# Kernel optimization log

Measured on AMD Instinct MI355X. Metric: run time of the kernel, lower is better.

The kernel has to match this reference:

```python
import jax, jax.numpy as jnp
import numpy as np
import math

H = 1024
NH = 16
D = H // NH  # 64
EPS = 1e-5


def _layernorm(x, g, b):
    mu = jnp.mean(x, axis=-1, keepdims=True)
    var = jnp.mean(jnp.square(x - mu), axis=-1, keepdims=True)
    return (x - mu) * jax.lax.rsqrt(var + EPS) * g + b


def setup_inputs() -> dict:
    key = jax.random.key(0)
    ks = jax.random.split(key, 12)
    B, T = 2, 2048
    q = jax.random.normal(ks[0], (B, T, H), jnp.float32)
    k = jax.random.normal(ks[1], (B, T, H), jnp.float32)
    v = jax.random.normal(ks[2], (B, T, H), jnp.float32)
    pad_mask = jax.random.randint(ks[3], (B, T), 0, 2) > 0
    s = 0.02
    Wq = jax.random.normal(ks[4], (H, H), jnp.float32) * s
    Wk = jax.random.normal(ks[5], (H, H), jnp.float32) * s
    Wv = jax.random.normal(ks[6], (H, H), jnp.float32) * s
    Wo = jax.random.normal(ks[7], (H, H), jnp.float32) * s
    W1 = jax.random.normal(ks[8], (4 * H, H), jnp.float32) * s
    b1 = jnp.zeros((4 * H,), jnp.float32)
    W2 = jax.random.normal(ks[9], (H, 4 * H), jnp.float32) * s
    b2 = jnp.zeros((H,), jnp.float32)
    g1 = jnp.ones((H,), jnp.float32); be1 = jnp.zeros((H,), jnp.float32)
    g2 = jnp.ones((H,), jnp.float32); be2 = jnp.zeros((H,), jnp.float32)
    return dict(q=q, k=k, v=v, pad_mask=pad_mask, Wq=Wq, Wk=Wk, Wv=Wv, Wo=Wo,
                W1=W1, b1=b1, W2=W2, b2=b2, g1=g1, be1=be1, g2=g2, be2=be2)


def reference(q, k, v, pad_mask, Wq, Wk, Wv, Wo, W1, b1, W2, b2, g1, be1, g2, be2):
    B, Tq, _ = q.shape
    Tv = v.shape[1]
    # torch nn.Linear: x @ W.T
    Q = (q @ Wq.T).reshape(B, NH, Tq, D)  # faithful to torch .view head split
    K = (k @ Wk.T).reshape(B, NH, Tv, D)
    V = (v @ Wv.T).reshape(B, NH, Tv, D)
    logits = jnp.einsum('baih,bajh->baij', Q, K)  # [B,NH,Tq,Tv]
    neg_inf = jnp.float32(-jnp.inf)
    logits = jnp.where(pad_mask[:, None, None, :], logits, neg_inf)
    attn = jax.nn.softmax(logits / math.sqrt(D), axis=-1)
    # post-softmax query-mask multiply (custom)
    attn = attn * pad_mask[:, None, :, None].astype(attn.dtype)
    h = jnp.einsum('baij,bajh->baih', attn, V).reshape(B, Tq, H)
    h = h @ Wo.T
    h = _layernorm(q + h, g1, be1)
    ff = jax.nn.gelu(h @ W1.T + b1, approximate=False) @ W2.T + b2  # dropout = identity (eval)
    return _layernorm(h + ff, g2, be2)
```

## Files before the change

### kernel.cpp

```cpp
#include <hip/hip_runtime.h>

typedef unsigned short u16;
typedef unsigned int u32;
typedef __attribute__((ext_vector_type(8))) __bf16 bf16x8;
typedef __attribute__((ext_vector_type(4))) float f32x4;
typedef __attribute__((ext_vector_type(16))) float f32x16;
typedef __attribute__((ext_vector_type(4))) unsigned short u16x4;
typedef __attribute__((ext_vector_type(8))) unsigned short u16x8;

#define LOG2E 1.44269504088896340736f

__device__ __forceinline__ u16 f2bf(float f) {
  union { float f; unsigned u; } c; c.f = f;
  unsigned r = c.u + 0x7FFFu + ((c.u >> 16) & 1u);
  return (u16)(r >> 16);
}
__device__ __forceinline__ float bf2f(u16 h) {
  union { unsigned u; float f; } c; c.u = ((unsigned)h) << 16;
  return c.f;
}

__device__ __forceinline__ void gload_lds16(const u16* g, u16* l) {
  __builtin_amdgcn_global_load_lds((const __attribute__((address_space(1))) unsigned int*)g,
                                   (__attribute__((address_space(3))) unsigned int*)l, 16, 0, 0);
}

__device__ __forceinline__ float gelu_fast(float x) {
  float z = fabsf(x) * 0.70710678118654752f;
  float t = 1.0f / (1.0f + 0.3275911f * z);
  float poly = t * (0.254829592f + t * (-0.284496736f + t * (1.421413741f +
               t * (-1.453152027f + t * 1.061405429f))));
  float e = __builtin_amdgcn_exp2f(-z * z * LOG2E);
  float erfz = 1.0f - poly * e;
  float s = (x >= 0.0f) ? erfz : -erfz;
  return 0.5f * x * (1.0f + s);
}

__global__ __launch_bounds__(256) void cvt_all(
    const float* __restrict__ s0, const float* __restrict__ s1, const float* __restrict__ s2,
    const float* __restrict__ s3, const float* __restrict__ s4, const float* __restrict__ s5,
    const float* __restrict__ s6, const float* __restrict__ s7, const float* __restrict__ s8,
    u16* __restrict__ d0, u16* __restrict__ d1, u16* __restrict__ d2,
    u16* __restrict__ d3, u16* __restrict__ d4, u16* __restrict__ d5,
    u16* __restrict__ d6, u16* __restrict__ d7, u16* __restrict__ d8) {
  int i = blockIdx.x * 256 + threadIdx.x;
  if (i >= 6291456) return;
  const float* src; u16* dst; int off;
  if (i < 3145728) {
    if (i < 1048576)      { src = s0; dst = d0; off = 0; }
    else if (i < 2097152) { src = s1; dst = d1; off = 1048576; }
    else                  { src = s2; dst = d2; off = 2097152; }
  } else if (i < 4194304) {
    if (i < 3407872)      { src = s3; dst = d3; off = 3145728; }
    else if (i < 3670016) { src = s4; dst = d4; off = 3407872; }
    else if (i < 3932160) { src = s5; dst = d5; off = 3670016; }
    else                  { src = s6; dst = d6; off = 3932160; }
  } else {
    if (i < 5242880)      { src = s7; dst = d7; off = 4194304; }
    else                  { src = s8; dst = d8; off = 5242880; }
  }
  int j = i - off;
  f32x4 v = ((const f32x4*)src)[j];
  u16x4 o;
  o[0] = f2bf(v[0]); o[1] = f2bf(v[1]); o[2] = f2bf(v[2]); o[3] = f2bf(v[3]);
  ((u16x4*)dst)[j] = o;
}

__global__ void build_masks(const void* __restrict__ pm, float* __restrict__ maskbias,
                            float* __restrict__ qmask, int n) {
  __shared__ int sflag;
  if (threadIdx.x == 0) sflag = 0;
  __syncthreads();
  const unsigned* pw = (const unsigned*)pm;
  int nwords = n / 4;
  int local = 0;
  for (int i = threadIdx.x; i < nwords; i += blockDim.x)
    if (pw[i] > 1u) local = 1;
  if (local) atomicOr(&sflag, 1);
  __syncthreads();
  bool isbool = (sflag != 0);
  for (int i = threadIdx.x; i < n; i += blockDim.x) {
    int m = isbool ? (int)((const unsigned char*)pm)[i] : ((const int*)pm)[i];
    maskbias[i] = m ? 0.0f : -2e30f;
    qmask[i]    = m ? 1.0f : 0.0f;
  }
}

template<int EPI>
__device__ __forceinline__ void gemm_core(const u16* __restrict__ A, const u16* __restrict__ Bw,
                                          const float* __restrict__ bias, u16* __restrict__ C,
                                          int N, int Kstride, int Klen, int bn, int bm, int tid) {
  __shared__ u16 smem[2][8192];
  int wave = tid >> 6, lane = tid & 63;
  int l15 = lane & 15, l4 = lane >> 4;
  int wr = (wave >> 1) * 64, wc = (wave & 1) * 64;
  int mrow0 = bm * 128, ncol0 = bn * 128;
  int srow = lane >> 2;
  int scol = (lane & 3) * 8;

  const u16* asrc0 = A  + (size_t)(mrow0 + (wave * 2 + 0) * 16 + srow) * Kstride + scol;
  const u16* asrc1 = A  + (size_t)(mrow0 + (wave * 2 + 1) * 16 + srow) * Kstride + scol;
  const u16* bsrc0 = Bw + (size_t)(ncol0 + (wave * 2 + 0) * 16 + srow) * Kstride + scol;
  const u16* bsrc1 = Bw + (size_t)(ncol0 + (wave * 2 + 1) * 16 + srow) * Kstride + scol;
  u16* ad0 = &smem[0][(wave * 2 + 0) * 512];
  u16* ad1 = &smem[0][(wave * 2 + 1) * 512];
  u16* bd0 = &smem[0][4096 + (wave * 2 + 0) * 512];
  u16* bd1 = &smem[0][4096 + (wave * 2 + 1) * 512];

  auto stage = [&](int buf, int k0) {
    gload_lds16(asrc0 + k0, ad0 + buf * 8192);
    gload_lds16(asrc1 + k0, ad1 + buf * 8192);
    gload_lds16(bsrc0 + k0, bd0 + buf * 8192);
    gload_lds16(bsrc1 + k0, bd1 + buf * 8192);
  };

  f32x4 acc[4][4];
#pragma unroll
  for (int i = 0; i < 4; i++)
#pragma unroll
    for (int j = 0; j < 4; j++) acc[i][j] = (f32x4)0.0f;

  int nsteps = Klen >> 5;
  stage(0, 0);
  for (int s = 0; s < nsteps; s++) {
    int cur = s & 1;
    __syncthreads();
    if (s + 1 < nsteps) stage(cur ^ 1, (s + 1) << 5);
    const u16* as = &smem[cur][0];
    const u16* bs = &smem[cur][4096];
    bf16x8 af[4], bfr[4];
#pragma unroll
    for (int mi = 0; mi < 4; mi++) af[mi]  = *(const bf16x8*)(as + (wr + mi * 16 + l15) * 32 + l4 * 8);
#pragma unroll
    for (int ni = 0; ni < 4; ni++) bfr[ni] = *(const bf16x8*)(bs + (wc + ni * 16 + l15) * 32 + l4 * 8);
#pragma unroll
    for (int mi = 0; mi < 4; mi++)
#pragma unroll
      for (int ni = 0; ni < 4; ni++)
        acc[mi][ni] = __builtin_amdgcn_mfma_f32_16x16x32_bf16(af[mi], bfr[ni], acc[mi][ni], 0, 0, 0);
  }

  u16* ct = &smem[0][0];
  for (int p = 0; p < 2; p++) {
    __syncthreads();
    if ((wave >> 1) == p) {
#pragma unroll
      for (int ni = 0; ni < 4; ni++) {
        int gcol = ncol0 + wc + ni * 16 + l15;
        float bv = (EPI > 0) ? bias[gcol] : 0.0f;
#pragma unroll
        for (int mi = 0; mi < 4; mi++) {
#pragma unroll
          for (int r = 0; r < 4; r++) {
            float v = acc[mi][ni][r] + bv;
            if (EPI == 2) v = gelu_fast(v);
            ct[(mi * 16 + l4 * 4 + r) * 136 + wc + ni * 16 + l15] = f2bf(v);
          }
        }
      }
    }
    __syncthreads();
    int lrow = tid >> 2, cq = tid & 3;
#pragma unroll
    for (int j = 0; j < 4; j++) {
      int col = cq * 8 + j * 32;
      u16x8 vv = *(const u16x8*)(ct + lrow * 136 + col);
      *(u16x8*)(C + (size_t)(mrow0 + p * 64 + lrow) * N + ncol0 + col) = vv;
    }
  }
}

template<int EPI>
__global__ __launch_bounds__(256) void gemm_bt(const u16* __restrict__ A, const u16* __restrict__ Bw,
                                               const float* __restrict__ bias, u16* __restrict__ C,
                                               int N, int K) {
  gemm_core<EPI>(A, Bw, bias, C, N, K, K, blockIdx.x, blockIdx.y, threadIdx.x);
}

__global__ __launch_bounds__(256) void gemm_splitk(const u16* __restrict__ A, const u16* __restrict__ Bw,
                                                   u16* __restrict__ P, int N, int Kstride, int Kc) {
  int z = blockIdx.z;
  size_t M = (size_t)gridDim.y * 128;
  gemm_core<0>(A + (size_t)z * Kc, Bw + (size_t)z * Kc, nullptr,
               P + (size_t)z * M * N, N, Kstride, Kc, blockIdx.x, blockIdx.y, threadIdx.x);
}

__global__ __launch_bounds__(256) void gemm_qkv(const u16* __restrict__ qb, const u16* __restrict__ kb,
                                                const u16* __restrict__ vb,
                                                const u16* __restrict__ wq, const u16* __restrict__ wk,
                                                const u16* __restrict__ wv,
                                                u16* __restrict__ Qo, u16* __restrict__ Ko, u16* __restrict__ Vo) {
  const u16* A; const u16* W; u16* C;
  if (blockIdx.z == 0)      { A = qb; W = wq; C = Qo; }
  else if (blockIdx.z == 1) { A = kb; W = wk; C = Ko; }
  else                      { A = vb; W = wv; C = Vo; }
  gemm_core<0>(A, W, nullptr, C, 1024, 1024, 1024, blockIdx.x, blockIdx.y, threadIdx.x);
}

__global__ __launch_bounds__(256) void transpose64(const u16* __restrict__ in, u16* __restrict__ out) {
  int bh = blockIdx.y, tb = blockIdx.x;
  __shared__ u16 tile[64 * 72];
  int tid = threadIdx.x;
#pragma unroll
  for (int it = 0; it < 2; it++) {
    int idx = it * 256 + tid;
    int r = idx >> 3, c8 = (idx & 7) * 8;
    u16x8 v = *(const u16x8*)(in + ((size_t)bh * 2048 + tb * 64 + r) * 64 + c8);
    int byte = ((r * 72 + c8) * 2) ^ (((r >> 3) & 7) << 4);
    *(u16x8*)((char*)tile + byte) = v;
  }
  __syncthreads();
#pragma unroll
  for (int it = 0; it < 2; it++) {
    int idx = it * 256 + tid;
    int d = idx >> 3, t8 = (idx & 7) * 8;
    u16x8 o;
#pragma unroll
    for (int e = 0; e < 8; e++) {
      int t = t8 + e;
      int byte = ((t * 72 + d) * 2) ^ (((t >> 3) & 7) << 4);
      o[e] = *(const u16*)((const char*)tile + byte);
    }
    *(u16x8*)(out + ((size_t)bh * 64 + d) * 2048 + tb * 64 + t8) = o;
  }
}

__global__ __launch_bounds__(256, 4) void attn4(const u16* __restrict__ Q, const u16* __restrict__ Kg,
                                                const u16* __restrict__ VT,
                                                const float* __restrict__ maskbias,
                                                u16* __restrict__ O0, u16* __restrict__ O1,
                                                float* __restrict__ Ms, float* __restrict__ Ss) {
  const int T = 2048;
  int bh = blockIdx.x;
  int qt = blockIdx.y;
  int sp = blockIdx.z;
  int b = bh >> 4;
  const u16* Qh = Q  + (size_t)bh * T * 64;
  const u16* Kh = Kg + (size_t)bh * T * 64;
  const u16* Vh = VT + (size_t)bh * T * 64;
  u16* Oh = (sp ? O1 : O0) + (size_t)bh * T * 64;
  const float* mb = maskbias + b * T + sp * 1024;
  int tid = threadIdx.x, w = tid >> 6, l = tid & 63;
  int q32 = l & 31, h = l >> 5;
  int qbase = qt * 128 + w * 32;
  const float C = 0.125f * LOG2E;

  __shared__ u16 Ks[2][4096];
  __shared__ u16 Vs[2][4096];

  bf16x8 qf[4];
#pragma unroll
  for (int dc = 0; dc < 4; dc++)
    qf[dc] = *(const bf16x8*)(Qh + (size_t)(qbase + q32) * 64 + dc * 16 + h * 8);

  int rl = l >> 3, ob = (l & 7) * 16;
  int osw = ob ^ (rl << 4);
  int r0 = w * 16 + rl, r1 = w * 16 + 8 + rl;
  const u16* pK0 = Kh + (size_t)(sp * 1024 + r0) * 64 + (osw >> 1);
  const u16* pK1 = Kh + (size_t)(sp * 1024 + r1) * 64 + (osw >> 1);
  const u16* pV0 = Vh + (size_t)r0 * 2048 + sp * 1024 + (osw >> 1);
  const u16* pV1 = Vh + (size_t)r1 * 2048 + sp * 1024 + (osw >> 1);
  u16* dK0 = &Ks[0][0] + (w * 16) * 64;
  u16* dK1 = &Ks[0][0] + (w * 16 + 8) * 64;
  u16* dV0 = &Vs[0][0] + (w * 16) * 64;
  u16* dV1 = &Vs[0][0] + (w * 16 + 8) * 64;

  auto stage = [&](int buf) {
    gload_lds16(pK0, dK0 + buf * 4096);
    gload_lds16(pK1, dK1 + buf * 4096);
    gload_lds16(pV0, dV0 + buf * 4096);
    gload_lds16(pV1, dV1 + buf * 4096);
    pK0 += 4096; pK1 += 4096; pV0 += 64; pV1 += 64;
  };

  f32x16 acc[2];
  acc[0] = (f32x16)0.0f; acc[1] = (f32x16)0.0f;
  float m_ = -3e30f, s_ = 0.0f;

  int swz = (q32 & 7) << 4;

  stage(0);
  for (int t = 0; t < 16; t++) {
    int cur = t & 1;
    __syncthreads();
    if (t < 15) stage(cur ^ 1);
    const char* ksb = (const char*)(&Ks[0][0] + cur * 4096);
    const char* vsb = (const char*)(&Vs[0][0] + cur * 4096);

    bf16x8 kf[2][4];
#pragma unroll
    for (int kvc = 0; kvc < 2; kvc++)
#pragma unroll
      for (int dc = 0; dc < 4; dc++)
        kf[kvc][dc] = *(const bf16x8*)(ksb + (kvc * 32 + q32) * 128 + ((dc * 32 + h * 16) ^ swz));

    f32x16 st[2];
    st[0] = (f32x16)0.0f; st[1] = (f32x16)0.0f;
#pragma unroll
    for (int kvc = 0; kvc < 2; kvc++)
#pragma unroll
      for (int dc = 0; dc < 4; dc++)
        st[kvc] = __builtin_amdgcn_mfma_f32_32x32x16_bf16(kf[kvc][dc], qf[dc], st[kvc], 0, 0, 0);

    float p[32];
    float pmax = -3e30f;
#pragma unroll
    for (int kvc = 0; kvc < 2; kvc++) {
#pragma unroll
      for (int g = 0; g < 4; g++) {
        f32x4 mv = *(const f32x4*)(mb + t * 64 + kvc * 32 + g * 8 + h * 4);
#pragma unroll
        for (int r = 0; r < 4; r++) {
          float val = st[kvc][g * 4 + r] * C + mv[r];
          p[kvc * 16 + g * 4 + r] = val;
          pmax = fmaxf(pmax, val);
        }
      }
    }
    pmax = fmaxf(pmax, __shfl_xor(pmax, 32));

    if (__any(pmax - m_ > 8.0f)) {
      float mnew = fmaxf(m_, pmax);
      float fsc = __builtin_amdgcn_exp2f(m_ - mnew);
      s_ *= fsc;
      m_ = mnew;
#pragma unroll
      for (int g = 0; g < 4; g++)
#pragma unroll
        for (int r = 0; r < 4; r++) {
          float f = __shfl(fsc, g * 8 + h * 4 + r);
          acc[0][g * 4 + r] *= f;
          acc[1][g * 4 + r] *= f;
        }
    }

    float rsum = 0.0f;
    u32 wds[16];
#pragma unroll
    for (int i = 0; i < 16; i++) {
      float a = __builtin_amdgcn_exp2f(p[2 * i] - m_);
      float bq = __builtin_amdgcn_exp2f(p[2 * i + 1] - m_);
      rsum += a + bq;
      union { __bf16 h2[2]; u32 u; } cv;
      cv.h2[0] = (__bf16)a; cv.h2[1] = (__bf16)bq;
      wds[i] = cv.u;
    }
    rsum += __shfl_xor(rsum, 32);
    s_ += rsum;

#pragma unroll
    for (int kvc = 0; kvc < 2; kvc++) {
      int bse = kvc * 8;
      u32 sw0 = __shfl_xor(wds[bse + 0], 32), sw1 = __shfl_xor(wds[bse + 1], 32);
      u32 sw2 = __shfl_xor(wds[bse + 2], 32), sw3 = __shfl_xor(wds[bse + 3], 32);
      u32 sw4 = __shfl_xor(wds[bse + 4], 32), sw5 = __shfl_xor(wds[bse + 5], 32);
      u32 sw6 = __shfl_xor(wds[bse + 6], 32), sw7 = __shfl_xor(wds[bse + 7], 32);
      union { u32 u[4]; bf16x8 v; } pa0, pa1;
      pa0.u[0] = h ? sw2 : wds[bse + 0];
      pa0.u[1] = h ? sw3 : wds[bse + 1];
      pa0.u[2] = h ? wds[bse + 2] : sw0;
      pa0.u[3] = h ? wds[bse + 3] : sw1;
      pa1.u[0] = h ? sw6 : wds[bse + 4];
      pa1.u[1] = h ? sw7 : wds[bse + 5];
      pa1.u[2] = h ? wds[bse + 6] : sw4;
      pa1.u[3] = h ? wds[bse + 7] : sw5;
#pragma unroll
      for (int cl = 0; cl < 2; cl++) {
        bf16x8 pa = cl ? pa1.v : pa0.v;
        int cg = kvc * 2 + cl;
#pragma unroll
        for (int dblk = 0; dblk < 2; dblk++) {
          bf16x8 vf = *(const bf16x8*)(vsb + (dblk * 32 + q32) * 128 + ((cg * 32 + h * 16) ^ swz));
          acc[dblk] = __builtin_amdgcn_mfma_f32_32x32x16_bf16(pa, vf, acc[dblk], 0, 0, 0);
        }
      }
    }
  }

#pragma unroll
  for (int g = 0; g < 4; g++) {
#pragma unroll
    for (int r = 0; r < 4; r++) {
      int row = g * 8 + h * 4 + r;
#pragma unroll
      for (int dblk = 0; dblk < 2; dblk++)
        Oh[(size_t)(qbase + row) * 64 + dblk * 32 + q32] = f2bf(acc[dblk][g * 4 + r]);
    }
  }
  if (h == 0) {
    int ro = sp * 65536 + bh * 2048 + qbase + q32;
    Ms[ro] = m_;
    Ss[ro] = s_;
  }
}

__global__ __launch_bounds__(256) void attn_combine(const u16* __restrict__ O0, const u16* __restrict__ O1,
                                                    const float* __restrict__ Ms, const float* __restrict__ Ss,
                                                    const float* __restrict__ qmaskf, u16* __restrict__ out) {
  int idx = blockIdx.x * 256 + threadIdx.x;
  int row = idx >> 3;
  int d8 = (idx & 7) * 8;
  int bh = row >> 11, r = row & 2047, b = bh >> 4;
  float m0 = Ms[row], m1 = Ms[65536 + row];
  float mstar = fmaxf(m0, m1);
  float w0 = __builtin_amdgcn_exp2f(m0 - mstar);
  float w1 = __builtin_amdgcn_exp2f(m1 - mstar);
  float den = w0 * Ss[row] + w1 * Ss[65536 + row];
  float scale = qmaskf[b * 2048 + r] / den;
  size_t base = (size_t)row * 64 + d8;
  u16x8 a0 = *(const u16x8*)(O0 + base);
  u16x8 a1 = *(const u16x8*)(O1 + base);
  u16x8 o;
#pragma unroll
  for (int e = 0; e < 8; e++)
    o[e] = f2bf((w0 * bf2f(a0[e]) + w1 * bf2f(a1[e])) * scale);
  *(u16x8*)(out + base) = o;
}

template<int NP, int A_F32, int ADD_BIAS, int OUT_F32>
__global__ __launch_bounds__(256) void add_ln_multi(const void* __restrict__ Ap,
                                                    const u16* __restrict__ P0, const u16* __restrict__ P1,
                                                    const u16* __restrict__ P2, const u16* __restrict__ P3,
                                                    const float* __restrict__ bias,
                                                    const float* __restrict__ g, const float* __restrict__ be,
                                                    void* __restrict__ outp) {
  int row = blockIdx.x, tid = threadIdx.x;
  int lane = tid & 63, wave = tid >> 6;
  size_t rb = (size_t)row * 1024;
  float x[4];
  if (A_F32) {
    f32x4 a = ((const f32x4*)((const float*)Ap + rb))[tid];
#pragma unroll
    for (int j = 0; j < 4; j++) x[j] = a[j];
  } else {
    u16x4 au = ((const u16x4*)((const u16*)Ap + rb))[tid];
#pragma unroll
    for (int j = 0; j < 4; j++) x[j] = bf2f(au[j]);
  }
  {
    u16x4 p = ((const u16x4*)(P0 + rb))[tid];
#pragma unroll
    for (int j = 0; j < 4; j++) x[j] += bf2f(p[j]);
  }
  if (NP > 1) {
    u16x4 p = ((const u16x4*)(P1 + rb))[tid];
#pragma unroll
    for (int j = 0; j < 4; j++) x[j] += bf2f(p[j]);
  }
  if (NP > 2) {
    u16x4 p = ((const u16x4*)(P2 + rb))[tid];
#pragma unroll
    for (int j = 0; j < 4; j++) x[j] += bf2f(p[j]);
  }
  if (NP > 3) {
    u16x4 p = ((const u16x4*)(P3 + rb))[tid];
#pragma unroll
    for (int j = 0; j < 4; j++) x[j] += bf2f(p[j]);
  }
  if (ADD_BIAS) {
    f32x4 bv = ((const f32x4*)bias)[tid];
#pragma unroll
    for (int j = 0; j < 4; j++) x[j] += bv[j];
  }
  float s = x[0] + x[1] + x[2] + x[3];
  float q = x[0] * x[0] + x[1] * x[1] + x[2] * x[2] + x[3] * x[3];
#pragma unroll
  for (int m = 1; m < 64; m <<= 1) { s += __shfl_xor(s, m); q += __shfl_xor(q, m); }
  __shared__ float rs[4], rq[4];
  if (lane == 0) { rs[wave] = s; rq[wave] = q; }
  __syncthreads();
  float S = rs[0] + rs[1] + rs[2] + rs[3];
  float Qq = rq[0] + rq[1] + rq[2] + rq[3];
  float mean = S * (1.0f / 1024.0f);
  float var = Qq * (1.0f / 1024.0f) - mean * mean;
  float rstd = rsqrtf(var + 1e-5f);
  if (OUT_F32) {
    f32x4 y;
#pragma unroll
    for (int j = 0; j < 4; j++) { int col = tid * 4 + j; y[j] = (x[j] - mean) * rstd * g[col] + be[col]; }
    ((f32x4*)((float*)outp + rb))[tid] = y;
  } else {
    u16x4 y;
#pragma unroll
    for (int j = 0; j < 4; j++) { int col = tid * 4 + j; y[j] = f2bf((x[j] - mean) * rstd * g[col] + be[col]); }
    ((u16x4*)((u16*)outp + rb))[tid] = y;
  }
}

extern "C" void kernel_launch(void* const* d_in, const int* in_sizes, int n_in,
                              void* d_out, int out_size, void* d_ws, size_t ws_size,
                              hipStream_t stream) {
  const float* q   = (const float*)d_in[0];
  const float* k   = (const float*)d_in[1];
  const float* v   = (const float*)d_in[2];
  const void*  pad = d_in[3];
  const float* Wq  = (const float*)d_in[4];
  const float* Wk  = (const float*)d_in[5];
  const float* Wv  = (const float*)d_in[6];
  const float* Wo  = (const float*)d_in[7];
  const float* W1  = (const float*)d_in[8];
  const float* b1  = (const float*)d_in[9];
  const float* W2  = (const float*)d_in[10];
  const float* b2  = (const float*)d_in[11];
  const float* g1  = (const float*)d_in[12];
  const float* be1 = (const float*)d_in[13];
  const float* g2  = (const float*)d_in[14];
  const float* be2 = (const float*)d_in[15];
  float* out = (float*)d_out;
  char* ws = (char*)d_ws;
  const size_t MB = 1u << 20;

  u16* wq_b = (u16*)(ws + 0 * MB);
  u16* wk_b = (u16*)(ws + 2 * MB);
  u16* wv_b = (u16*)(ws + 4 * MB);
  u16* wo_b = (u16*)(ws + 6 * MB);
  u16* w1_b = (u16*)(ws + 8 * MB);
  u16* w2_b = (u16*)(ws + 16 * MB);
  u16* qb   = (u16*)(ws + 24 * MB);
  u16* kb   = (u16*)(ws + 32 * MB);
  u16* vb   = (u16*)(ws + 40 * MB);
  u16* Qb   = (u16*)(ws + 48 * MB);
  u16* Kb   = (u16*)(ws + 56 * MB);
  u16* Vb   = (u16*)(ws + 64 * MB);
  u16* VTb  = (u16*)(ws + 72 * MB);
  u16* hatt = (u16*)(ws + 80 * MB);
  u16* Op0  = (u16*)(ws + 24 * MB);
  u16* Op1  = (u16*)(ws + 32 * MB);
  float* Ms = (float*)(ws + 88 * MB);
  float* Ss = (float*)(ws + 89 * MB);
  u16* WP   = (u16*)(ws + 40 * MB);
  u16* h1b  = (u16*)(ws + 24 * MB);
  u16* ff1  = (u16*)(ws + 32 * MB);
  u16* Fp   = (u16*)(ws + 64 * MB);
  float* maskbias = (float*)(ws + 96 * MB);
  float* qmaskf   = (float*)(ws + 96 * MB + 16384);

  build_masks<<<1, 256, 0, stream>>>(pad, maskbias, qmaskf, in_sizes[3]);

  cvt_all<<<24576, 256, 0, stream>>>(q, k, v, Wq, Wk, Wv, Wo, W1, W2,
                                     qb, kb, vb, wq_b, wk_b, wv_b, wo_b, w1_b, w2_b);

  gemm_qkv<<<dim3(8, 32, 3), 256, 0, stream>>>(qb, kb, vb, wq_b, wk_b, wv_b, Qb, Kb, Vb);

  transpose64<<<dim3(32, 32), 256, 0, stream>>>(Vb, VTb);

  attn4<<<dim3(32, 16, 2), 256, 0, stream>>>(Qb, Kb, VTb, maskbias, Op0, Op1, Ms, Ss);

  attn_combine<<<2048, 256, 0, stream>>>(Op0, Op1, Ms, Ss, qmaskf, hatt);

  gemm_splitk<<<dim3(8, 32, 2), 256, 0, stream>>>(hatt, wo_b, WP, 1024, 1024, 512);

  add_ln_multi<2, 1, 0, 0><<<4096, 256, 0, stream>>>(q, WP, WP + 4194304, nullptr, nullptr,
                                                     nullptr, g1, be1, h1b);

  gemm_bt<2><<<dim3(32, 32), 256, 0, stream>>>(h1b, w1_b, b1, ff1, 4096, 1024);

  gemm_splitk<<<dim3(8, 32, 4), 256, 0, stream>>>(ff1, w2_b, Fp, 1024, 4096, 1024);

  add_ln_multi<4, 0, 1, 1><<<4096, 256, 0, stream>>>(h1b, Fp, Fp + 4194304, Fp + 2 * 4194304,
                                                     Fp + 3 * 4194304, b2, g2, be2, out);
}
```

Measured before the change: 307.2 us.

## Remap GEMM blocks across XCDs, tune barriers, use permlane swaps and bf16 mask in attention

Several independent tweaks land together. GEMM kernels remap the linear block index so that neighbouring tiles share an XCD for L2 reuse, gain a min-occupancy launch bound, and replace the loop barrier with an explicit vmcnt wait plus s_barrier. The attention kernel stores the mask bias as bf16 and prefetches it into registers one iteration ahead, computes the row max as a tree of three-way maxes, and swaps the cross-half shuffles for permlane32_swap. Together these aim to cut cache misses, synchronisation and shuffle overhead. A bf16 copy of -2e30 is still a large negative number, so masking keeps working.

```diff
diff --git a/kernel.cpp b/kernel.cpp
--- a/kernel.cpp
+++ b/kernel.cpp
@@ -7,6 +7,7 @@
 typedef __attribute__((ext_vector_type(16))) float f32x16;
 typedef __attribute__((ext_vector_type(4))) unsigned short u16x4;
 typedef __attribute__((ext_vector_type(8))) unsigned short u16x8;
+typedef __attribute__((ext_vector_type(2))) int i32x2;
 
 #define LOG2E 1.44269504088896340736f
 
@@ -19,10 +20,25 @@
   union { unsigned u; float f; } c; c.u = ((unsigned)h) << 16;
   return c.f;
 }
+__device__ __forceinline__ float max3f(float a, float b, float c) {
+  return fmaxf(fmaxf(a, b), c);
+}
 
 __device__ __forceinline__ void gload_lds16(const u16* g, u16* l) {
   __builtin_amdgcn_global_load_lds((const __attribute__((address_space(1))) unsigned int*)g,
                                    (__attribute__((address_space(3))) unsigned int*)l, 16, 0, 0);
+}
+
+__device__ __forceinline__ void xcd_remap(int& bn, int& bm, int& bz) {
+  int gx = gridDim.x, gxy = gridDim.x * gridDim.y;
+  int lin = blockIdx.z * gxy + blockIdx.y * gx + blockIdx.x;
+  int nwg = gxy * gridDim.z;
+  int q = nwg >> 3;
+  int w = (lin & 7) * q + (lin >> 3);
+  bz = w / gxy;
+  int rem = w - bz * gxy;
+  bm = rem / gx;
+  bn = rem - bm * gx;
 }
 
 __device__ __forceinline__ float gelu_fast(float x) {
@@ -66,7 +82,7 @@
   ((u16x4*)dst)[j] = o;
 }
 
-__global__ void build_masks(const void* __restrict__ pm, float* __restrict__ maskbias,
+__global__ void build_masks(const void* __restrict__ pm, u16* __restrict__ mask16,
                             float* __restrict__ qmask, int n) {
   __shared__ int sflag;
   if (threadIdx.x == 0) sflag = 0;
@@ -81,8 +97,8 @@
   bool isbool = (sflag != 0);
   for (int i = threadIdx.x; i < n; i += blockDim.x) {
     int m = isbool ? (int)((const unsigned char*)pm)[i] : ((const int*)pm)[i];
-    maskbias[i] = m ? 0.0f : -2e30f;
-    qmask[i]    = m ? 1.0f : 0.0f;
+    mask16[i] = f2bf(m ? 0.0f : -2e30f);
+    qmask[i]  = m ? 1.0f : 0.0f;
   }
 }
 
@@ -123,11 +139,11 @@
   int nsteps = Klen >> 5;
   stage(0, 0);
   for (int s = 0; s < nsteps; s++) {
-    int cur = s & 1;
-    __syncthreads();
-    if (s + 1 < nsteps) stage(cur ^ 1, (s + 1) << 5);
-    const u16* as = &smem[cur][0];
-    const u16* bs = &smem[cur][4096];
+    asm volatile("s_waitcnt vmcnt(0)" ::: "memory");
+    __builtin_amdgcn_s_barrier();
+    if (s + 1 < nsteps) stage((s + 1) & 1, (s + 1) << 5);
+    const u16* as = &smem[s & 1][0];
+    const u16* bs = &smem[s & 1][4096];
     bf16x8 af[4], bfr[4];
 #pragma unroll
     for (int mi = 0; mi < 4; mi++) af[mi]  = *(const bf16x8*)(as + (wr + mi * 16 + l15) * 32 + l4 * 8);
@@ -140,9 +156,10 @@
         acc[mi][ni] = __builtin_amdgcn_mfma_f32_16x16x32_bf16(af[mi], bfr[ni], acc[mi][ni], 0, 0, 0);
   }
 
+  __syncthreads();
   u16* ct = &smem[0][0];
   for (int p = 0; p < 2; p++) {
-    __syncthreads();
+    if (p) __syncthreads();
     if ((wave >> 1) == p) {
 #pragma unroll
       for (int ni = 0; ni < 4; ni++) {
@@ -171,30 +188,35 @@
 }
 
 template<int EPI>
-__global__ __launch_bounds__(256) void gemm_bt(const u16* __restrict__ A, const u16* __restrict__ Bw,
-                                               const float* __restrict__ bias, u16* __restrict__ C,
-                                               int N, int K) {
-  gemm_core<EPI>(A, Bw, bias, C, N, K, K, blockIdx.x, blockIdx.y, threadIdx.x);
-}
-
-__global__ __launch_bounds__(256) void gemm_splitk(const u16* __restrict__ A, const u16* __restrict__ Bw,
-                                                   u16* __restrict__ P, int N, int Kstride, int Kc) {
-  int z = blockIdx.z;
+__global__ __launch_bounds__(256, 3) void gemm_bt(const u16* __restrict__ A, const u16* __restrict__ Bw,
+                                                  const float* __restrict__ bias, u16* __restrict__ C,
+                                                  int N, int K) {
+  int bn, bm, bz;
+  xcd_remap(bn, bm, bz);
+  gemm_core<EPI>(A, Bw, bias, C, N, K, K, bn, bm, threadIdx.x);
+}
+
+__global__ __launch_bounds__(256, 3) void gemm_splitk(const u16* __restrict__ A, const u16* __restrict__ Bw,
+                                                      u16* __restrict__ P, int N, int Kstride, int Kc) {
+  int bn, bm, bz;
+  xcd_remap(bn, bm, bz);
   size_t M = (size_t)gridDim.y * 128;
-  gemm_core<0>(A + (size_t)z * Kc, Bw + (size_t)z * Kc, nullptr,
-               P + (size_t)z * M * N, N, Kstride, Kc, blockIdx.x, blockIdx.y, threadIdx.x);
-}
-
-__global__ __launch_bounds__(256) void gemm_qkv(const u16* __restrict__ qb, const u16* __restrict__ kb,
-                                                const u16* __restrict__ vb,
-                                                const u16* __restrict__ wq, const u16* __restrict__ wk,
-                                                const u16* __restrict__ wv,
-                                                u16* __restrict__ Qo, u16* __restrict__ Ko, u16* __restrict__ Vo) {
+  gemm_core<0>(A + (size_t)bz * Kc, Bw + (size_t)bz * Kc, nullptr,
+               P + (size_t)bz * M * N, N, Kstride, Kc, bn, bm, threadIdx.x);
+}
+
+__global__ __launch_bounds__(256, 3) void gemm_qkv(const u16* __restrict__ qb, const u16* __restrict__ kb,
+                                                   const u16* __restrict__ vb,
+                                                   const u16* __restrict__ wq, const u16* __restrict__ wk,
+                                                   const u16* __restrict__ wv,
+                                                   u16* __restrict__ Qo, u16* __restrict__ Ko, u16* __restrict__ Vo) {
+  int bn, bm, bz;
+  xcd_remap(bn, bm, bz);
   const u16* A; const u16* W; u16* C;
-  if (blockIdx.z == 0)      { A = qb; W = wq; C = Qo; }
-  else if (blockIdx.z == 1) { A = kb; W = wk; C = Ko; }
-  else                      { A = vb; W = wv; C = Vo; }
-  gemm_core<0>(A, W, nullptr, C, 1024, 1024, 1024, blockIdx.x, blockIdx.y, threadIdx.x);
+  if (bz == 0)      { A = qb; W = wq; C = Qo; }
+  else if (bz == 1) { A = kb; W = wk; C = Ko; }
+  else              { A = vb; W = wv; C = Vo; }
+  gemm_core<0>(A, W, nullptr, C, 1024, 1024, 1024, bn, bm, threadIdx.x);
 }
 
 __global__ __launch_bounds__(256) void transpose64(const u16* __restrict__ in, u16* __restrict__ out) {
@@ -227,7 +249,7 @@
 
 __global__ __launch_bounds__(256, 4) void attn4(const u16* __restrict__ Q, const u16* __restrict__ Kg,
                                                 const u16* __restrict__ VT,
-                                                const float* __restrict__ maskbias,
+                                                const u16* __restrict__ mask16,
                                                 u16* __restrict__ O0, u16* __restrict__ O1,
                                                 float* __restrict__ Ms, float* __restrict__ Ss) {
   const int T = 2048;
@@ -239,7 +261,7 @@
   const u16* Kh = Kg + (size_t)bh * T * 64;
   const u16* Vh = VT + (size_t)bh * T * 64;
   u16* Oh = (sp ? O1 : O0) + (size_t)bh * T * 64;
-  const float* mb = maskbias + b * T + sp * 1024;
+  const u16* mb = mask16 + b * T + sp * 1024;
   int tid = threadIdx.x, w = tid >> 6, l = tid & 63;
   int q32 = l & 31, h = l >> 5;
   int qbase = qt * 128 + w * 32;
@@ -279,6 +301,13 @@
 
   int swz = (q32 & 7) << 4;
 
+  u16x4 mvv[2][4];
+#pragma unroll
+  for (int kvc = 0; kvc < 2; kvc++)
+#pragma unroll
+    for (int g = 0; g < 4; g++)
+      mvv[kvc][g] = *(const u16x4*)(mb + kvc * 32 + g * 8 + h * 4);
+
   stage(0);
   for (int t = 0; t < 16; t++) {
     int cur = t & 1;
@@ -303,21 +332,25 @@
         st[kvc] = __builtin_amdgcn_mfma_f32_32x32x16_bf16(kf[kvc][dc], qf[dc], st[kvc], 0, 0, 0);
 
     float p[32];
-    float pmax = -3e30f;
 #pragma unroll
     for (int kvc = 0; kvc < 2; kvc++) {
 #pragma unroll
       for (int g = 0; g < 4; g++) {
-        f32x4 mv = *(const f32x4*)(mb + t * 64 + kvc * 32 + g * 8 + h * 4);
-#pragma unroll
-        for (int r = 0; r < 4; r++) {
-          float val = st[kvc][g * 4 + r] * C + mv[r];
-          p[kvc * 16 + g * 4 + r] = val;
-          pmax = fmaxf(pmax, val);
-        }
+#pragma unroll
+        for (int r = 0; r < 4; r++)
+          p[kvc * 16 + g * 4 + r] = st[kvc][g * 4 + r] * C + bf2f(mvv[kvc][g][r]);
       }
     }
-    pmax = fmaxf(pmax, __shfl_xor(pmax, 32));
+    float ma = p[0], mb2 = p[16];
+#pragma unroll
+    for (int i = 0; i < 7; i++) {
+      ma  = max3f(ma,  p[1 + 2 * i],  p[2 + 2 * i]);
+      mb2 = max3f(mb2, p[17 + 2 * i], p[18 + 2 * i]);
+    }
+    ma = fmaxf(ma, p[15]); mb2 = fmaxf(mb2, p[31]);
+    float pmax = fmaxf(ma, mb2);
+    i32x2 pr = __builtin_amdgcn_permlane32_swap(__float_as_int(pmax), __float_as_int(pmax), false, false);
+    pmax = fmaxf(__int_as_float(pr[0]), __int_as_float(pr[1]));
 
     if (__any(pmax - m_ > 8.0f)) {
       float mnew = fmaxf(m_, pmax);
@@ -345,25 +378,20 @@
       cv.h2[0] = (__bf16)a; cv.h2[1] = (__bf16)bq;
       wds[i] = cv.u;
     }
-    rsum += __shfl_xor(rsum, 32);
+    i32x2 sr = __builtin_amdgcn_permlane32_swap(__float_as_int(rsum), __float_as_int(rsum), false, false);
+    rsum = __int_as_float(sr[0]) + __int_as_float(sr[1]);
     s_ += rsum;
 
 #pragma unroll
     for (int kvc = 0; kvc < 2; kvc++) {
       int bse = kvc * 8;
-      u32 sw0 = __shfl_xor(wds[bse + 0], 32), sw1 = __shfl_xor(wds[bse + 1], 32);
-      u32 sw2 = __shfl_xor(wds[bse + 2], 32), sw3 = __shfl_xor(wds[bse + 3], 32);
-      u32 sw4 = __shfl_xor(wds[bse + 4], 32), sw5 = __shfl_xor(wds[bse + 5], 32);
-      u32 sw6 = __shfl_xor(wds[bse + 6], 32), sw7 = __shfl_xor(wds[bse + 7], 32);
+      i32x2 r02 = __builtin_amdgcn_permlane32_swap((int)wds[bse + 0], (int)wds[bse + 2], false, false);
+      i32x2 r13 = __builtin_amdgcn_permlane32_swap((int)wds[bse + 1], (int)wds[bse + 3], false, false);
+      i32x2 r46 = __builtin_amdgcn_permlane32_swap((int)wds[bse + 4], (int)wds[bse + 6], false, false);
+      i32x2 r57 = __builtin_amdgcn_permlane32_swap((int)wds[bse + 5], (int)wds[bse + 7], false, false);
       union { u32 u[4]; bf16x8 v; } pa0, pa1;
-      pa0.u[0] = h ? sw2 : wds[bse + 0];
-      pa0.u[1] = h ? sw3 : wds[bse + 1];
-      pa0.u[2] = h ? wds[bse + 2] : sw0;
-      pa0.u[3] = h ? wds[bse + 3] : sw1;
-      pa1.u[0] = h ? sw6 : wds[bse + 4];
-      pa1.u[1] = h ? sw7 : wds[bse + 5];
-      pa1.u[2] = h ? wds[bse + 6] : sw4;
-      pa1.u[3] = h ? wds[bse + 7] : sw5;
+      pa0.u[0] = (u32)r02[0]; pa0.u[1] = (u32)r13[0]; pa0.u[2] = (u32)r02[1]; pa0.u[3] = (u32)r13[1];
+      pa1.u[0] = (u32)r46[0]; pa1.u[1] = (u32)r57[0]; pa1.u[2] = (u32)r46[1]; pa1.u[3] = (u32)r57[1];
 #pragma unroll
       for (int cl = 0; cl < 2; cl++) {
         bf16x8 pa = cl ? pa1.v : pa0.v;
@@ -374,6 +402,14 @@
           acc[dblk] = __builtin_amdgcn_mfma_f32_32x32x16_bf16(pa, vf, acc[dblk], 0, 0, 0);
         }
       }
+    }
+
+    if (t < 15) {
+#pragma unroll
+      for (int kvc = 0; kvc < 2; kvc++)
+#pragma unroll
+        for (int g = 0; g < 4; g++)
+          mvv[kvc][g] = *(const u16x4*)(mb + (t + 1) * 64 + kvc * 32 + g * 8 + h * 4);
     }
   }
 
@@ -532,10 +568,10 @@
   u16* h1b  = (u16*)(ws + 24 * MB);
   u16* ff1  = (u16*)(ws + 32 * MB);
   u16* Fp   = (u16*)(ws + 64 * MB);
-  float* maskbias = (float*)(ws + 96 * MB);
-  float* qmaskf   = (float*)(ws + 96 * MB + 16384);
-
-  build_masks<<<1, 256, 0, stream>>>(pad, maskbias, qmaskf, in_sizes[3]);
+  u16* mask16   = (u16*)(ws + 96 * MB);
+  float* qmaskf = (float*)(ws + 96 * MB + 16384);
+
+  build_masks<<<1, 256, 0, stream>>>(pad, mask16, qmaskf, in_sizes[3]);
 
   cvt_all<<<24576, 256, 0, stream>>>(q, k, v, Wq, Wk, Wv, Wo, W1, W2,
                                      qb, kb, vb, wq_b, wk_b, wv_b, wo_b, w1_b, w2_b);
@@ -544,7 +580,7 @@
 
   transpose64<<<dim3(32, 32), 256, 0, stream>>>(Vb, VTb);
 
-  attn4<<<dim3(32, 16, 2), 256, 0, stream>>>(Qb, Kb, VTb, maskbias, Op0, Op1, Ms, Ss);
+  attn4<<<dim3(32, 16, 2), 256, 0, stream>>>(Qb, Kb, VTb, mask16, Op0, Op1, Ms, Ss);
 
   attn_combine<<<2048, 256, 0, stream>>>(Op0, Op1, Ms, Ss, qmaskf, hatt);
 
```

Result: faster. 282.6 us (-8.0%).
